# Performance work log

Measured on AMD Instinct MI355X. Metric: run time of the kernel, lower is better.

## Reference

```python
import jax, jax.numpy as jnp
from jax import lax
import numpy as np

EPSILON = 0.5
BETA = 1.0
N_ITER_FREE = 500
N_ITER_CLAMPED = 8


def setup_inputs() -> dict:
    key = jax.random.key(0)
    ks = jax.random.split(key, 12)
    B = 256
    x = jax.random.uniform(ks[0], (B, 784), dtype=jnp.float32)
    t = jax.random.uniform(ks[1], (B, 10), dtype=jnp.float32)
    u1 = jnp.zeros((B, 500), jnp.float32)
    u2 = jnp.zeros((B, 500), jnp.float32)
    u3 = jnp.zeros((B, 500), jnp.float32)
    u4 = jnp.zeros((B, 10), jnp.float32)
    a0 = np.float32(np.sqrt(2.0 / (784.0 + 500.0)))
    a1 = np.float32(np.sqrt(2.0 / (500.0 + 500.0)))
    a2 = np.float32(np.sqrt(2.0 / (500.0 + 10.0)))
    W0 = jax.random.normal(ks[2], (784, 500), jnp.float32) * a0
    b0 = jax.random.normal(ks[3], (500,), jnp.float32) * a0
    W1 = jax.random.normal(ks[4], (500, 500), jnp.float32) * a1
    b1 = jax.random.normal(ks[5], (500,), jnp.float32) * a1
    W2 = jax.random.normal(ks[6], (500, 500), jnp.float32) * a1
    b2 = jax.random.normal(ks[7], (500,), jnp.float32) * a1
    W3 = jax.random.normal(ks[8], (500, 10), jnp.float32) * a2
    b3 = jax.random.normal(ks[9], (10,), jnp.float32) * a2
    return dict(x=x, u1=u1, u2=u2, u3=u3, u4=u4, t=t,
                W0=W0, W1=W1, W2=W2, W3=W3, b0=b0, b1=b1, b2=b2, b3=b3)


def _rho(v):
    return jnp.clip(v, 0.0, 1.0)


def _d_rho(v):
    return ((v >= 0.0) & (v <= 1.0)).astype(v.dtype)


def reference(x, u1, u2, u3, u4, t, W0, W1, W2, W3, b0, b1, b2, b3):
    # x (units[0]) is clamped input; precompute its constant drive into layer 1.
    xW0 = x @ W0 + b0  # [B,500], invariant across iterations

    def deltas(c):
        u1, u2, u3, u4 = c
        # Jacobi update: all d_units use the pre-update states (matches torch code).
        d1 = _d_rho(u1) * (xW0 + u2 @ W1.T) - u1
        d2 = _d_rho(u2) * (u1 @ W1 + u3 @ W2.T + b1) - u2
        d3 = _d_rho(u3) * (u2 @ W2 + u4 @ W3.T + b2) - u3
        d4 = _d_rho(u4) * (u3 @ W3 + b3) - u4
        return d1, d2, d3, d4

    def free_step(c, _):
        d1, d2, d3, d4 = deltas(c)
        new = tuple(_rho(u + EPSILON * d) for u, d in zip(c, (d1, d2, d3, d4)))
        return new, None

    def clamped_step(c, _):
        d1, d2, d3, d4 = deltas(c)
        d4 = d4 + BETA * (t - c[3])
        new = tuple(_rho(u + EPSILON * d) for u, d in zip(c, (d1, d2, d3, d4)))
        return new, None

    units_free, _ = lax.scan(free_step, (u1, u2, u3, u4), None, length=N_ITER_FREE)
    units_clamped, _ = lax.scan(clamped_step, units_free, None, length=N_ITER_CLAMPED)
    # fixed_points returns (units_free, units_clamped); flatten the two phases.
    return (*units_free, *units_clamped)
```

## Files before the change

kernel.cpp:

```cpp
#include <hip/hip_runtime.h>


typedef float  f32x4 __attribute__((ext_vector_type(4)));
typedef short  s16x8 __attribute__((ext_vector_type(8)));
typedef short  s16x4 __attribute__((ext_vector_type(4)));
typedef unsigned int uint;
typedef uint   u32x4 __attribute__((ext_vector_type(4)));

#define MFMA_BF16 __builtin_amdgcn_mfma_f32_16x16x32_bf16

#define NFREE   500
#define NCLAMP  8
#define NITER   (NFREE + NCLAMP)
#define ROWLEN  1568
#define NSAMP   256
#define ROWTOT  (NSAMP * ROWLEN)

#define B1_OFF   0
#define B2A_OFF  262144
#define B2B_OFF  524288
#define B3A_OFF  786432
#define B3B_OFF  1048576
#define B4_OFF   1064960
#define BTOT     1081344

#define WS_UHL   0
#define WS_XW0   (WS_UHL + 2*ROWTOT*4)
#define WS_BIAS  (WS_XW0 + NSAMP*512*4)
#define WS_CNT   (WS_BIAS + 6400)
#define WS_BH    (WS_CNT + 1024)
#define WS_BL    (WS_BH + BTOT*2)
#define WS_END   (WS_BL + BTOT*2)

__device__ __forceinline__ short f2bf(float f){
  unsigned u = __float_as_uint(f);
  unsigned r = (u + 0x7FFFu + ((u >> 16) & 1u)) >> 16;
  return (short)r;
}
__device__ __forceinline__ float bf2f(short s){
  return __uint_as_float(((unsigned)(unsigned short)s) << 16);
}
__device__ __forceinline__ uint packbf(float v){
  short h = f2bf(v);
  short l = f2bf(v - bf2f(h));
  return (uint)(unsigned short)h | ((uint)(unsigned short)l << 16);
}

#define SYSLD(dst, addr) \
  asm volatile("global_load_dwordx4 %0, %1, off sc0 sc1" : "=v"(dst) : "v"(addr) : "memory")
__device__ __forceinline__ void store_sys(uint* p, uint v){
  asm volatile("global_store_dword %0, %1, off sc0 sc1" :: "v"(p), "v"(v) : "memory");
}
#define WAITALL() do { \
  asm volatile("s_waitcnt vmcnt(0)" ::: "memory"); \
  __builtin_amdgcn_sched_barrier(0); } while(0)
#define UNPK(X, OFF) do { \
  s16x4 h_ = (s16x4){ (short)((X)[0] & 0xffff), (short)((X)[1] & 0xffff), \
                      (short)((X)[2] & 0xffff), (short)((X)[3] & 0xffff) }; \
  s16x4 l_ = (s16x4){ (short)((X)[0] >> 16), (short)((X)[1] >> 16), \
                      (short)((X)[2] >> 16), (short)((X)[3] >> 16) }; \
  *(s16x4*)(L + (OFF)) = h_; *(s16x4*)(L + 32768 + (OFF)) = l_; } while(0)

#define BARRIER(ITV) do { \
  asm volatile("s_waitcnt vmcnt(0)" ::: "memory"); \
  __syncthreads(); \
  if (tid == 0){ \
    __hip_atomic_fetch_add(cg, 1u, __ATOMIC_RELAXED, __HIP_MEMORY_SCOPE_SYSTEM); \
    const unsigned tgt_ = 16u * (unsigned)((ITV) + 1); \
    while (__hip_atomic_load(cg, __ATOMIC_RELAXED, __HIP_MEMORY_SCOPE_SYSTEM) < tgt_){ \
      __builtin_amdgcn_s_sleep(1); \
    } \
  } \
  __syncthreads(); } while(0)

__global__ void initK(const float* __restrict__ u1, const float* __restrict__ u2,
                      const float* __restrict__ u3, const float* __restrict__ u4,
                      const float* __restrict__ b1, const float* __restrict__ b2,
                      uint* __restrict__ uhl, float* __restrict__ bias,
                      uint* __restrict__ cnt){
  const int b = blockIdx.x, tid = threadIdx.x;
  for (int col = tid; col < ROWLEN; col += 256){
    float v;
    if      (col < 512)  v = (col < 500)        ? u1[b*500 + col]        : 0.f;
    else if (col < 1024) v = ((col-512) < 500)  ? u2[b*500 + col - 512]  : 0.f;
    else if (col < 1536) v = ((col-1024) < 500) ? u3[b*500 + col - 1024] : 0.f;
    else                 v = ((col-1536) < 10)  ? u4[b*10 + col - 1536]  : 0.f;
    uhl[b*ROWLEN + col] = packbf(v);
    if (b == 0){
      float bv = 0.f;
      if      (col >= 512  && col < 1024){ int i = col-512;  if (i < 500) bv = b1[i]; }
      else if (col >= 1024 && col < 1536){ int i = col-1024; if (i < 500) bv = b2[i]; }
      bias[col] = bv;
    }
  }
  if (b == 0) cnt[tid] = 0;
}

__global__ void xw0K(const float* __restrict__ x, const float* __restrict__ W0,
                     const float* __restrict__ b0, float* __restrict__ xw0p){
  __shared__ float xs[784];
  const int b = blockIdx.x, tid = threadIdx.x;
  for (int j = tid; j < 784; j += 512) xs[j] = x[b*784 + j];
  __syncthreads();
  float a = 0.f;
  if (tid < 500){
    a = b0[tid];
    #pragma unroll 4
    for (int j = 0; j < 784; ++j) a = fmaf(xs[j], W0[j*500 + tid], a);
  }
  xw0p[b*512 + tid] = (tid < 500) ? a : 0.f;
}

__global__ void packK(const float* __restrict__ W1, const float* __restrict__ W2,
                      const float* __restrict__ W3, short* __restrict__ Bh,
                      short* __restrict__ Bl){
  const int bid = blockIdx.x, ln = threadIdx.x;
  int m, base, nks, poff;
  if      (bid < 512) { m=0; base=0;    nks=16; poff=B1_OFF;  }
  else if (bid < 1024){ m=1; base=512;  nks=16; poff=B2A_OFF; }
  else if (bid < 1536){ m=2; base=1024; nks=16; poff=B2B_OFF; }
  else if (bid < 2048){ m=3; base=1536; nks=16; poff=B3A_OFF; }
  else if (bid < 2080){ m=4; base=2048; nks=1;  poff=B3B_OFF; }
  else                { m=5; base=2080; nks=16; poff=B4_OFF;  }
  const int local = bid - base, ct = local / nks, ks = local % nks;
  short hv[8], lv[8];
  #pragma unroll
  for (int j = 0; j < 8; ++j){
    const int k = ks*32 + (ln>>4)*8 + j;
    const int c = ct*16 + (ln & 15);
    float v = 0.f;
    if      (m==0){ if (k<500 && c<500) v = W1[c*500 + k]; }
    else if (m==1){ if (k<500 && c<500) v = W1[k*500 + c]; }
    else if (m==2){ if (k<500 && c<500) v = W2[c*500 + k]; }
    else if (m==3){ if (k<500 && c<500) v = W2[k*500 + c]; }
    else if (m==4){ if (k<10  && c<500) v = W3[c*10  + k]; }
    else          { if (k<500 && c<10 ) v = W3[k*10  + c]; }
    short h = f2bf(v); hv[j] = h; lv[j] = f2bf(v - bf2f(h));
  }
  const int o = poff + (ct*nks + ks)*512 + ln*8;
  #pragma unroll
  for (int j = 0; j < 8; ++j){ Bh[o+j] = hv[j]; Bl[o+j] = lv[j]; }
}

__global__ void __launch_bounds__(256, 1) mainK(
    const short* __restrict__ Bh, const short* __restrict__ Bl,
    uint* __restrict__ uhl, const float* __restrict__ xw0p,
    const float* __restrict__ bias,
    const float* __restrict__ u1in, const float* __restrict__ u2in,
    const float* __restrict__ u3in, const float* __restrict__ u4in,
    const float* __restrict__ tin, const float* __restrict__ b3,
    float* __restrict__ dout, uint* __restrict__ cnt)
{
  __shared__ short ldss[32768];
  char* L = (char*)ldss;
  const int bid = blockIdx.x;
  const int rg  = bid & 15;
  const int tp  = bid >> 4;
  const int tid = threadIdx.x;
  const int wv  = tid >> 6, ln = tid & 63;
  const int lrow = ln & 15, lkg = ln >> 4;
  const int rowbase = rg * 16;
  const int sg16 = tid >> 4, l16 = tid & 15;
  const int abase = lrow*2048 + ((lkg*16) ^ ((lrow & 7) << 4));
  uint* cg = cnt + rg*16;

  if (tp < 8){
    s16x8 bh[32], bl[32];
    const int ctg = tp*4 + wv;
    #pragma unroll
    for (int ks = 0; ks < 32; ++ks){
      const int of = (ks < 16 ? B2A_OFF + (ctg*16 + ks)*512
                              : B2B_OFF + (ctg*16 + ks - 16)*512) + ln*8;
      bh[ks] = *(const s16x8*)(Bh + of);
      bl[ks] = *(const s16x8*)(Bl + of);
    }
    const int i0 = tp*64 + wv*16 + lrow;
    const int colg = 512 + i0;
    const float biasv = bias[colg];
    f32x4 uold, uold4;
    #pragma unroll
    for (int r = 0; r < 4; ++r){
      const int b = rowbase + lkg*4 + r;
      uold[r]  = (i0 < 500)   ? u2in[b*500 + i0]  : 0.f;
      uold4[r] = (lrow < 10)  ? u4in[b*10 + lrow] : 0.f;
    }
    const int rA = sg16 >> 1, half = sg16 & 1;
    const bool doU4 = (tp == 0 && wv == 0);

    for (int it = 0; it < NITER; ++it){
      const uint* uhlB = uhl + (size_t)(it & 1)*ROWTOT;
      uint*       uhlN = uhl + (size_t)((it & 1) ^ 1)*ROWTOT;
      const int snap = (it == NFREE-1) ? 0 : ((it == NITER-1) ? 386560 : -1);
      {
        const uint* sA = uhlB + (size_t)(rowbase + rA)*ROWLEN + half*1024 + l16*4;
        const uint* sB = sA + 8*ROWLEN;
        u32x4 a0,a1,a2,a3,a4,a5,a6,a7,c0,c1,c2,c3,c4,c5,c6,c7;
        SYSLD(a0, sA+0);   SYSLD(a1, sA+64);  SYSLD(a2, sA+128); SYSLD(a3, sA+192);
        SYSLD(a4, sA+256); SYSLD(a5, sA+320); SYSLD(a6, sA+384); SYSLD(a7, sA+448);
        SYSLD(c0, sB+0);   SYSLD(c1, sB+64);  SYSLD(c2, sB+128); SYSLD(c3, sB+192);
        SYSLD(c4, sB+256); SYSLD(c5, sB+320); SYSLD(c6, sB+384); SYSLD(c7, sB+448);
        WAITALL();
        const int obA = rA*2048 + ((half*1024 + l16*8) ^ ((rA & 7) << 4));
        const int obB = obA + 16384;
        UNPK(a0, obA+0);   UNPK(a1, obA+128); UNPK(a2, obA+256); UNPK(a3, obA+384);
        UNPK(a4, obA+512); UNPK(a5, obA+640); UNPK(a6, obA+768); UNPK(a7, obA+896);
        UNPK(c0, obB+0);   UNPK(c1, obB+128); UNPK(c2, obB+256); UNPK(c3, obB+384);
        UNPK(c4, obB+512); UNPK(c5, obB+640); UNPK(c6, obB+768); UNPK(c7, obB+896);
      }
      __syncthreads();
      f32x4 h4 = {0.f,0.f,0.f,0.f}, x4 = {0.f,0.f,0.f,0.f};
      if (doU4){
        #pragma unroll
        for (int ks = 0; ks < 16; ++ks){
          const int off = (abase + 1024) ^ (ks*64);
          s16x8 aH = *(const s16x8*)(L + off);
          s16x8 aL = *(const s16x8*)(L + 32768 + off);
          const int of4 = B4_OFF + ks*512 + ln*8;
          s16x8 b4h = *(const s16x8*)(Bh + of4);
          s16x8 b4l = *(const s16x8*)(Bl + of4);
          h4 = MFMA_BF16(aH, b4h, h4, 0, 0, 0);
          x4 = MFMA_BF16(aH, b4l, x4, 0, 0, 0);
          x4 = MFMA_BF16(aL, b4h, x4, 0, 0, 0);
        }
      }
      f32x4 acch = {0.f,0.f,0.f,0.f}, accx = {0.f,0.f,0.f,0.f};
      #pragma unroll
      for (int ks = 0; ks < 32; ++ks){
        const int off = abase ^ (ks*64);
        s16x8 aH = *(const s16x8*)(L + off);
        s16x8 aL = *(const s16x8*)(L + 32768 + off);
        acch = MFMA_BF16(aH, bh[ks], acch, 0, 0, 0);
        accx = MFMA_BF16(aH, bl[ks], accx, 0, 0, 0);
        accx = MFMA_BF16(aL, bh[ks], accx, 0, 0, 0);
      }
      #pragma unroll
      for (int r = 0; r < 4; ++r){
        const int b = rowbase + lkg*4 + r;
        const float y = acch[r] + accx[r] + biasv;
        float v = 0.5f*(uold[r] + y);
        v = fminf(fmaxf(v, 0.f), 1.f);
        if (i0 >= 500) v = 0.f;
        uold[r] = v;
        store_sys(uhlN + (size_t)b*ROWLEN + colg, packbf(v));
        if (snap >= 0 && i0 < 500) dout[snap + 128000 + b*500 + i0] = v;
      }
      if (doU4){
        const bool clamped = (it >= NFREE);
        #pragma unroll
        for (int r = 0; r < 4; ++r){
          const int b = rowbase + lkg*4 + r;
          float v = 0.f;
          if (lrow < 10){
            const float y = h4[r] + x4[r] + b3[lrow];
            v = clamped ? 0.5f*(y + tin[b*10 + lrow]) : 0.5f*(uold4[r] + y);
            v = fminf(fmaxf(v, 0.f), 1.f);
          }
          uold4[r] = v;
          store_sys(uhlN + (size_t)b*ROWLEN + 1536 + lrow, packbf(v));
          store_sys(uhlN + (size_t)b*ROWLEN + 1552 + lrow, 0u);
          if (snap >= 0 && lrow < 10) dout[snap + 384000 + b*10 + lrow] = v;
        }
      }
      BARRIER(it);
    }
  } else {
    const bool IS3 = (tp >= 12);
    const int cbb  = IS3 ? (tp - 12) : (tp - 8);
    const int ct0  = cbb*8 + wv*2;
    s16x8 bh0[16], bl0[16], bh1[16], bl1[16];
    {
      const int base = IS3 ? B3A_OFF : B1_OFF;
      #pragma unroll
      for (int ks = 0; ks < 16; ++ks){
        const int ofA = base + ((ct0+0)*16 + ks)*512 + ln*8;
        const int ofB = base + ((ct0+1)*16 + ks)*512 + ln*8;
        bh0[ks] = *(const s16x8*)(Bh + ofA); bl0[ks] = *(const s16x8*)(Bl + ofA);
        bh1[ks] = *(const s16x8*)(Bh + ofB); bl1[ks] = *(const s16x8*)(Bl + ofB);
      }
    }
    s16x8 th0 = {0,0,0,0,0,0,0,0}, tl0 = th0, th1 = th0, tl1 = th0;
    if (IS3){
      th0 = *(const s16x8*)(Bh + B3B_OFF + (ct0+0)*512 + ln*8);
      tl0 = *(const s16x8*)(Bl + B3B_OFF + (ct0+0)*512 + ln*8);
      th1 = *(const s16x8*)(Bh + B3B_OFF + (ct0+1)*512 + ln*8);
      tl1 = *(const s16x8*)(Bl + B3B_OFF + (ct0+1)*512 + ln*8);
    }
    const int colg0 = (IS3 ? 1024 : 0) + cbb*128 + wv*32;
    const int iA = (colg0 & 511) + lrow, iB = iA + 16;
    const float biasA = bias[colg0 + lrow], biasB = bias[colg0 + 16 + lrow];
    const float* uin = IS3 ? u3in : u1in;
    f32x4 uoldA, uoldB;
    #pragma unroll
    for (int r = 0; r < 4; ++r){
      const int b = rowbase + lkg*4 + r;
      uoldA[r] = (iA < 500) ? uin[b*500 + iA] : 0.f;
      uoldB[r] = (iB < 500) ? uin[b*500 + iB] : 0.f;
    }
    const int dseg = IS3 ? 256000 : 0;

    for (int it = 0; it < NITER; ++it){
      const uint* uhlB = uhl + (size_t)(it & 1)*ROWTOT;
      uint*       uhlN = uhl + (size_t)((it & 1) ^ 1)*ROWTOT;
      const int snap = (it == NFREE-1) ? 0 : ((it == NITER-1) ? 386560 : -1);
      {
        const uint* sA = uhlB + (size_t)(rowbase + sg16)*ROWLEN + 512 + l16*4;
        u32x4 a0,a1,a2,a3,a4,a5,a6,a7, c0;
        SYSLD(a0, sA+0);   SYSLD(a1, sA+64);  SYSLD(a2, sA+128); SYSLD(a3, sA+192);
        SYSLD(a4, sA+256); SYSLD(a5, sA+320); SYSLD(a6, sA+384); SYSLD(a7, sA+448);
        const int row4 = tid >> 3, q = tid & 7;
        if (tid < 128)
          SYSLD(c0, uhlB + (size_t)(rowbase + row4)*ROWLEN + 1536 + q*4);
        WAITALL();
        const int ob = sg16*2048 + ((l16*8) ^ ((sg16 & 7) << 4));
        UNPK(a0, ob+0);   UNPK(a1, ob+128); UNPK(a2, ob+256); UNPK(a3, ob+384);
        UNPK(a4, ob+512); UNPK(a5, ob+640); UNPK(a6, ob+768); UNPK(a7, ob+896);
        if (tid < 128){
          const int ob4 = row4*2048 + ((1024 + q*8) ^ ((row4 & 7) << 4));
          UNPK(c0, ob4);
        }
      }
      __syncthreads();
      f32x4 hA = {0.f,0.f,0.f,0.f}, xA = {0.f,0.f,0.f,0.f};
      f32x4 hB = {0.f,0.f,0.f,0.f}, xB = {0.f,0.f,0.f,0.f};
      #pragma unroll
      for (int ks = 0; ks < 16; ++ks){
        const int off = abase ^ (ks*64);
        s16x8 aH = *(const s16x8*)(L + off);
        s16x8 aL = *(const s16x8*)(L + 32768 + off);
        hA = MFMA_BF16(aH, bh0[ks], hA, 0, 0, 0);
        xA = MFMA_BF16(aH, bl0[ks], xA, 0, 0, 0);
        xA = MFMA_BF16(aL, bh0[ks], xA, 0, 0, 0);
        hB = MFMA_BF16(aH, bh1[ks], hB, 0, 0, 0);
        xB = MFMA_BF16(aH, bl1[ks], xB, 0, 0, 0);
        xB = MFMA_BF16(aL, bh1[ks], xB, 0, 0, 0);
      }
      if (IS3){
        const int off = abase + 1024;
        s16x8 aH = *(const s16x8*)(L + off);
        s16x8 aL = *(const s16x8*)(L + 32768 + off);
        hA = MFMA_BF16(aH, th0, hA, 0, 0, 0);
        xA = MFMA_BF16(aH, tl0, xA, 0, 0, 0);
        xA = MFMA_BF16(aL, th0, xA, 0, 0, 0);
        hB = MFMA_BF16(aH, th1, hB, 0, 0, 0);
        xB = MFMA_BF16(aH, tl1, xB, 0, 0, 0);
        xB = MFMA_BF16(aL, th1, xB, 0, 0, 0);
      }
      #pragma unroll
      for (int r = 0; r < 4; ++r){
        const int b = rowbase + lkg*4 + r;
        {
          float y = hA[r] + xA[r] + biasA;
          if (!IS3) y += xw0p[b*512 + colg0 + lrow];
          float v = 0.5f*(uoldA[r] + y);
          v = fminf(fmaxf(v, 0.f), 1.f);
          if (iA >= 500) v = 0.f;
          uoldA[r] = v;
          store_sys(uhlN + (size_t)b*ROWLEN + colg0 + lrow, packbf(v));
          if (snap >= 0 && iA < 500) dout[snap + dseg + b*500 + iA] = v;
        }
        {
          float y = hB[r] + xB[r] + biasB;
          if (!IS3) y += xw0p[b*512 + colg0 + 16 + lrow];
          float v = 0.5f*(uoldB[r] + y);
          v = fminf(fmaxf(v, 0.f), 1.f);
          if (iB >= 500) v = 0.f;
          uoldB[r] = v;
          store_sys(uhlN + (size_t)b*ROWLEN + colg0 + 16 + lrow, packbf(v));
          if (snap >= 0 && iB < 500) dout[snap + dseg + b*500 + iB] = v;
        }
      }
      BARRIER(it);
    }
  }
}

extern "C" void kernel_launch(void* const* d_in, const int* in_sizes, int n_in,
                              void* d_out, int out_size, void* d_ws, size_t ws_size,
                              hipStream_t stream)
{
  const float* x  = (const float*)d_in[0];
  const float* u1 = (const float*)d_in[1];
  const float* u2 = (const float*)d_in[2];
  const float* u3 = (const float*)d_in[3];
  const float* u4 = (const float*)d_in[4];
  const float* t  = (const float*)d_in[5];
  const float* W0 = (const float*)d_in[6];
  const float* W1 = (const float*)d_in[7];
  const float* W2 = (const float*)d_in[8];
  const float* W3 = (const float*)d_in[9];
  const float* b0 = (const float*)d_in[10];
  const float* b1 = (const float*)d_in[11];
  const float* b2 = (const float*)d_in[12];
  const float* b3 = (const float*)d_in[13];

  char* ws = (char*)d_ws;
  uint*  uhl  = (uint*) (ws + WS_UHL);
  float* xw0p = (float*)(ws + WS_XW0);
  float* bias = (float*)(ws + WS_BIAS);
  uint*  cnt  = (uint*) (ws + WS_CNT);
  short* Bh   = (short*)(ws + WS_BH);
  short* Bl   = (short*)(ws + WS_BL);
  float* dout = (float*)d_out;

  initK<<<256, 256, 0, stream>>>(u1, u2, u3, u4, b1, b2, uhl, bias, cnt);
  xw0K<<<256, 512, 0, stream>>>(x, W0, b0, xw0p);
  packK<<<2112, 64, 0, stream>>>(W1, W2, W3, Bh, Bl);

  void* args[] = { &Bh, &Bl, &uhl, &xw0p, &bias,
                   &u1, &u2, &u3, &u4, &t, &b3, &dout, &cnt };
  hipError_t e = hipLaunchCooperativeKernel((const void*)mainK, dim3(256),
                                            dim3(256), args, 0, stream);
  if (e != hipSuccess){
    mainK<<<256, 256, 0, stream>>>(Bh, Bl, uhl, xw0p, bias,
                                   u1, u2, u3, u4, t, b3, dout, cnt);
  }
  (void)in_sizes; (void)n_in; (void)out_size; (void)ws_size;
}
```

Measured before the change: 3.996 ms.

## Replace per-iteration full group barrier with bipartite producer/consumer flags

The 16-block all-to-all spin barrier per row group is split into two counters, one for the even-layer (u2/u4) blocks and one for the odd-layer (u1/u3) blocks. Each side signals after writing and waits only for its partner side's count before reading the next state. This works because layer updates only read the opposite parity's states, so blocks no longer stall on same-parity peers and the two halves can drift by one iteration. The cost is that all threads now poll the partner counter instead of a single lane, and the counter region is doubled in the workspace.

```diff
diff --git a/kernel.cpp b/kernel.cpp
--- a/kernel.cpp
+++ b/kernel.cpp
@@ -28,7 +28,7 @@
 #define WS_XW0   (WS_UHL + 2*ROWTOT*4)
 #define WS_BIAS  (WS_XW0 + NSAMP*512*4)
 #define WS_CNT   (WS_BIAS + 6400)
-#define WS_BH    (WS_CNT + 1024)
+#define WS_BH    (WS_CNT + 2048)
 #define WS_BL    (WS_BH + BTOT*2)
 #define WS_END   (WS_BL + BTOT*2)
 
@@ -61,17 +61,21 @@
                       (short)((X)[2] >> 16), (short)((X)[3] >> 16) }; \
   *(s16x4*)(L + (OFF)) = h_; *(s16x4*)(L + 32768 + (OFF)) = l_; } while(0)
 
-#define BARRIER(ITV) do { \
+#define WAIT_PARTNER(ITV) do { \
+  if ((ITV) > 0){ \
+    const uint tgt_ = 8u * (uint)(ITV); \
+    while (__hip_atomic_load(other, __ATOMIC_RELAXED, \
+                             __HIP_MEMORY_SCOPE_SYSTEM) < tgt_) \
+      __builtin_amdgcn_s_sleep(1); \
+  } \
+} while(0)
+#define SIGNAL_MINE() do { \
   asm volatile("s_waitcnt vmcnt(0)" ::: "memory"); \
   __syncthreads(); \
-  if (tid == 0){ \
-    __hip_atomic_fetch_add(cg, 1u, __ATOMIC_RELAXED, __HIP_MEMORY_SCOPE_SYSTEM); \
-    const unsigned tgt_ = 16u * (unsigned)((ITV) + 1); \
-    while (__hip_atomic_load(cg, __ATOMIC_RELAXED, __HIP_MEMORY_SCOPE_SYSTEM) < tgt_){ \
-      __builtin_amdgcn_s_sleep(1); \
-    } \
-  } \
-  __syncthreads(); } while(0)
+  if (tid == 0) \
+    __hip_atomic_fetch_add(mine, 1u, __ATOMIC_RELAXED, \
+                           __HIP_MEMORY_SCOPE_SYSTEM); \
+} while(0)
 
 __global__ void initK(const float* __restrict__ u1, const float* __restrict__ u2,
                       const float* __restrict__ u3, const float* __restrict__ u4,
@@ -93,7 +97,7 @@
       bias[col] = bv;
     }
   }
-  if (b == 0) cnt[tid] = 0;
+  if (b == 0){ cnt[tid] = 0; cnt[tid + 256] = 0; }
 }
 
 __global__ void xw0K(const float* __restrict__ x, const float* __restrict__ W0,
@@ -162,9 +166,11 @@
   const int rowbase = rg * 16;
   const int sg16 = tid >> 4, l16 = tid & 15;
   const int abase = lrow*2048 + ((lkg*16) ^ ((lrow & 7) << 4));
-  uint* cg = cnt + rg*16;
-
-  if (tp < 8){
+  const bool isU2 = (tp < 8);
+  uint* mine  = cnt + rg*32 + (isU2 ? 0 : 16);
+  uint* other = cnt + rg*32 + (isU2 ? 16 : 0);
+
+  if (isU2){
     s16x8 bh[32], bl[32];
     const int ctg = tp*4 + wv;
     #pragma unroll
@@ -191,6 +197,7 @@
       const uint* uhlB = uhl + (size_t)(it & 1)*ROWTOT;
       uint*       uhlN = uhl + (size_t)((it & 1) ^ 1)*ROWTOT;
       const int snap = (it == NFREE-1) ? 0 : ((it == NITER-1) ? 386560 : -1);
+      WAIT_PARTNER(it);
       {
         const uint* sA = uhlB + (size_t)(rowbase + rA)*ROWLEN + half*1024 + l16*4;
         const uint* sB = sA + 8*ROWLEN;
@@ -261,7 +268,7 @@
           if (snap >= 0 && lrow < 10) dout[snap + 384000 + b*10 + lrow] = v;
         }
       }
-      BARRIER(it);
+      SIGNAL_MINE();
     }
   } else {
     const bool IS3 = (tp >= 12);
@@ -302,6 +309,7 @@
       const uint* uhlB = uhl + (size_t)(it & 1)*ROWTOT;
       uint*       uhlN = uhl + (size_t)((it & 1) ^ 1)*ROWTOT;
       const int snap = (it == NFREE-1) ? 0 : ((it == NITER-1) ? 386560 : -1);
+      WAIT_PARTNER(it);
       {
         const uint* sA = uhlB + (size_t)(rowbase + sg16)*ROWLEN + 512 + l16*4;
         u32x4 a0,a1,a2,a3,a4,a5,a6,a7, c0;
@@ -369,7 +377,7 @@
           if (snap >= 0 && iB < 500) dout[snap + dseg + b*500 + iB] = v;
         }
       }
-      BARRIER(it);
+      SIGNAL_MINE();
     }
   }
 }
```

Result: slower. 4.128 ms (+3.3%).
